# Kernel tuning notes

Hardware: AMD Instinct MI355X
Metric: run time of the kernel (lower is better)

## Reference

```python
import jax, jax.numpy as jnp
import numpy as np

N_NODES = 50000
N_EDGES = 800000
IN_DIM = 128
HID = 128
N_GRAPHS = 256
N_CLASSES = 2
ALPHA = 0.2  # leaky relu slope
EPS_BN = 1e-5


def setup_inputs() -> dict:
    key = jax.random.key(0)
    ks = jax.random.split(key, 24)
    adjacency = jax.random.randint(ks[0], (2, N_EDGES), 0, N_NODES, dtype=jnp.int32)
    input_feature = jax.random.normal(ks[1], (N_NODES, IN_DIM), dtype=jnp.float32)
    graph_indicator = jnp.sort(jax.random.randint(ks[2], (N_NODES,), 0, N_GRAPHS, dtype=jnp.int32))
    labels = jax.random.randint(ks[3], (N_GRAPHS,), 0, N_CLASSES, dtype=jnp.int64)
    s = 0.05
    params = {
        'W1': jax.random.normal(ks[4], (IN_DIM, HID), jnp.float32) * s,
        'a1': jax.random.normal(ks[5], (2 * HID,), jnp.float32) * s,
        'bn2_g': jnp.ones((HID,), jnp.float32),
        'bn2_b': jnp.zeros((HID,), jnp.float32),
        'W2': jax.random.normal(ks[6], (HID, HID), jnp.float32) * s,
        'a2': jax.random.normal(ks[7], (2 * HID,), jnp.float32) * s,
        'bn3_g': jnp.ones((HID,), jnp.float32),
        'bn3_b': jnp.zeros((HID,), jnp.float32),
        'W3': jax.random.normal(ks[8], (HID, HID), jnp.float32) * s,
        'a3': jax.random.normal(ks[9], (2 * HID,), jnp.float32) * s,
        'fc1_w': jax.random.normal(ks[10], (HID, 2 * HID), jnp.float32) * s,
        'fc1_b': jnp.zeros((2 * HID,), jnp.float32),
        'fc2_w': jax.random.normal(ks[11], (2 * HID, HID), jnp.float32) * s,
        'fc2_b': jnp.zeros((HID,), jnp.float32),
        'fc3_w': jax.random.normal(ks[12], (HID, N_CLASSES), jnp.float32) * s,
        'fc3_b': jnp.zeros((N_CLASSES,), jnp.float32),
    }
    return dict(adjacency=adjacency, input_feature=input_feature,
                graph_indicator=graph_indicator, labels=labels, **params)


def _batchnorm(x, g, b):
    # training-mode BatchNorm1d over node dim (biased variance)
    mu = jnp.mean(x, axis=0)
    var = jnp.mean((x - mu) ** 2, axis=0)
    return (x - mu) * jax.lax.rsqrt(var + EPS_BN) * g + b


def _sp_gat(x, src, dst, W, a):
    # pyGAT SpGraphAttentionLayer (dropout disabled / eval mode)
    h = x @ W                                # [N, F]
    F = h.shape[1]
    e_src = h @ a[:F]                        # [N]
    e_dst = h @ a[F:]                        # [N]
    e = e_src[src] + e_dst[dst]              # [E]
    ee = jnp.exp(-jax.nn.leaky_relu(e, ALPHA))
    rowsum = jax.ops.segment_sum(ee, src, num_segments=N_NODES)          # [N]
    num = jax.ops.segment_sum(ee[:, None] * h[dst], src, num_segments=N_NODES)  # [N, F]
    h_prime = num / (rowsum[:, None] + 1e-16)
    return jax.nn.elu(h_prime)


def reference(adjacency, input_feature, graph_indicator, labels,
              W1, a1, bn2_g, bn2_b, W2, a2, bn3_g, bn3_b, W3, a3,
              fc1_w, fc1_b, fc2_w, fc2_b, fc3_w, fc3_b):
    src, dst = adjacency[0], adjacency[1]
    # bn1 output is discarded in the original forward
    x = _sp_gat(input_feature, src, dst, W1, a1)
    x = _batchnorm(x, bn2_g, bn2_b)
    x = _sp_gat(x, src, dst, W2, a2)
    x = _batchnorm(x, bn3_g, bn3_b)
    x = _sp_gat(x, src, dst, W3, a3)
    # pooling_sum_4tensor: per-graph sum pooling
    pooled = jax.ops.segment_sum(x, graph_indicator, num_segments=N_GRAPHS)  # [G, F]
    x = jax.nn.relu(pooled @ fc1_w + fc1_b)
    x = jax.nn.relu(x @ fc2_w + fc2_b)
    logits = x @ fc3_w + fc3_b
    return logits
```

## Files before the change

kernel.cpp:

```cpp
#include <hip/hip_runtime.h>
#include <hip/hip_bf16.h>

#define N_NODES 50000
#define N_EDGES 800000
#define FD 128
#define N_GRAPHS 256
#define NPART 6250

typedef unsigned short u16;
typedef short bf16x8 __attribute__((ext_vector_type(8)));
typedef float f32x4 __attribute__((ext_vector_type(4)));

__device__ __forceinline__ u16 f2bf(float v) {
    __hip_bfloat16 h = __float2bfloat16(v);
    union { __hip_bfloat16 hh; u16 u; } c; c.hh = h; return c.u;
}
__device__ __forceinline__ float bf2f(u16 r) {
    return __uint_as_float(((unsigned int)r) << 16);
}

__global__ __launch_bounds__(256) void count_deg_part_k(const int* __restrict__ src,
                                                        int* __restrict__ cnt, int E) {
    int part = blockIdx.x & 7;
    int lo = part * NPART, hi = lo + NPART;
    int stride = (gridDim.x >> 3) * 256;
    for (int e = (blockIdx.x >> 3) * 256 + threadIdx.x; e < E; e += stride) {
        int s = src[e];
        if (s >= lo && s < hi) atomicAdd(&cnt[s], 1);
    }
}

__global__ __launch_bounds__(256) void fill_csr_part_k(const int* __restrict__ src,
                                                       const int* __restrict__ dst,
                                                       int* __restrict__ cur,
                                                       int* __restrict__ edst, int E) {
    int part = blockIdx.x & 7;
    int lo = part * NPART, hi = lo + NPART;
    int stride = (gridDim.x >> 3) * 256;
    for (int e = (blockIdx.x >> 3) * 256 + threadIdx.x; e < E; e += stride) {
        int s = src[e];
        if (s >= lo && s < hi) {
            int p = atomicAdd(&cur[s], 1);
            edst[p] = dst[e];
        }
    }
}

__global__ __launch_bounds__(256) void scan1_k(const int* __restrict__ cnt,
                                               int* __restrict__ bsum, int M,
                                               float* __restrict__ bnbuf,
                                               float* __restrict__ pooled) {
    int i = blockIdx.x * 256 + threadIdx.x;
    int v = (i < M) ? cnt[i] : 0;
    __shared__ int l[256];
    l[threadIdx.x] = v;
    __syncthreads();
    for (int s = 128; s > 0; s >>= 1) {
        if (threadIdx.x < s) l[threadIdx.x] += l[threadIdx.x + s];
        __syncthreads();
    }
    if (threadIdx.x == 0) bsum[blockIdx.x] = l[0];
    if (blockIdx.x == 0) {
        bnbuf[threadIdx.x] = 0.f; bnbuf[threadIdx.x + 256] = 0.f;
        for (int k = threadIdx.x; k < N_GRAPHS * FD; k += 256) pooled[k] = 0.f;
    }
}

__global__ __launch_bounds__(256) void scan3_k(const int* __restrict__ cnt,
                                               const int* __restrict__ bsum,
                                               int* __restrict__ offs,
                                               int* __restrict__ cur, int M, int NB) {
    int i = blockIdx.x * 256 + threadIdx.x;
    int tid = threadIdx.x;
    __shared__ int bs[256];
    bs[tid] = (tid < NB) ? bsum[tid] : 0;
    __syncthreads();
    for (int off = 1; off < 256; off <<= 1) {
        int t = (tid >= off) ? bs[tid - off] : 0;
        __syncthreads();
        bs[tid] += t;
        __syncthreads();
    }
    int base = (blockIdx.x == 0) ? 0 : bs[blockIdx.x - 1];
    int v = (i < M) ? cnt[i] : 0;
    __shared__ int l[256];
    l[tid] = v;
    __syncthreads();
    for (int off = 1; off < 256; off <<= 1) {
        int t = (tid >= off) ? l[tid - off] : 0;
        __syncthreads();
        l[tid] += t;
        __syncthreads();
    }
    int excl = l[tid] - v + base;
    if (i < M) { offs[i] = excl; cur[i] = excl; }
    if (i == M - 1) offs[M] = excl + v;
}

__global__ __launch_bounds__(128) void wprep1_k(const float* __restrict__ W,
                                                u16* __restrict__ Wt,
                                                float* __restrict__ cvec) {
    int n = blockIdx.x, k = threadIdx.x;
    Wt[(size_t)n * FD + k] = f2bf(W[(size_t)k * FD + n]);
    if (k == 0) cvec[n] = 0.f;
}

__global__ __launch_bounds__(128) void bnfw_k(const float* __restrict__ W,
                                              const float* __restrict__ sums,
                                              const float* __restrict__ sumsq,
                                              const float* __restrict__ g,
                                              const float* __restrict__ b,
                                              float invN,
                                              u16* __restrict__ Wt,
                                              float* __restrict__ cvec) {
    int n = blockIdx.x, k = threadIdx.x;
    __shared__ float scs[128], shs[128], l[128];
    float mu = sums[k] * invN;
    float var = sumsq[k] * invN - mu * mu;
    float sc = g[k] * rsqrtf(var + 1e-5f);
    scs[k] = sc;
    shs[k] = b[k] - mu * sc;
    __syncthreads();
    float w = W[(size_t)k * FD + n];
    Wt[(size_t)n * FD + k] = f2bf(scs[k] * w);
    l[k] = shs[k] * w;
    __syncthreads();
    for (int s = 64; s > 0; s >>= 1) {
        if (k < s) l[k] += l[k + s];
        __syncthreads();
    }
    if (k == 0) cvec[n] = l[0];
}

__global__ __launch_bounds__(256) void gemm_mfma_k(const float* __restrict__ Xf,
                                                   const u16* __restrict__ Xb,
                                                   int use_f32,
                                                   const u16* __restrict__ Wt,
                                                   const float* __restrict__ cvec,
                                                   const float* __restrict__ avec,
                                                   u16* __restrict__ Hb,
                                                   float* __restrict__ es,
                                                   float* __restrict__ ed, int M) {
    __shared__ u16 As[64][136];
    __shared__ u16 Bs[128][136];
    __shared__ float sa_s[128], sa_d[128], cv[128];
    int tid = threadIdx.x;
    if (tid < 128) { sa_s[tid] = avec[tid]; sa_d[tid] = avec[128 + tid]; cv[tid] = cvec[tid]; }
    int row0 = blockIdx.x * 64;
    {
        int n = tid >> 1, k0 = (tid & 1) * 64;
        const uint4* s = (const uint4*)(Wt + (size_t)n * FD + k0);
#pragma unroll
        for (int u = 0; u < 8; u++) *(uint4*)&Bs[n][k0 + u * 8] = s[u];
    }
    {
        int r = tid >> 2, k0 = (tid & 3) * 32;
        int grow = row0 + r;
        if (grow < M) {
            if (use_f32) {
                const float4* s = (const float4*)(Xf + (size_t)grow * FD + k0);
#pragma unroll
                for (int u = 0; u < 8; u++) {
                    float4 v = s[u];
                    ushort4 o;
                    o.x = f2bf(v.x); o.y = f2bf(v.y); o.z = f2bf(v.z); o.w = f2bf(v.w);
                    *(ushort4*)&As[r][k0 + u * 4] = o;
                }
            } else {
                const uint4* s = (const uint4*)(Xb + (size_t)grow * FD + k0);
#pragma unroll
                for (int u = 0; u < 4; u++) *(uint4*)&As[r][k0 + u * 8] = s[u];
            }
        } else {
            uint4 z = make_uint4(0, 0, 0, 0);
#pragma unroll
            for (int u = 0; u < 4; u++) *(uint4*)&As[r][k0 + u * 8] = z;
        }
    }
    __syncthreads();

    int wave = tid >> 6, lane = tid & 63;
    int quad = lane >> 4, n16 = lane & 15;
    int rbase = wave * 16;
    f32x4 acc[8];
    f32x4 zz = {0.f, 0.f, 0.f, 0.f};
#pragma unroll
    for (int t = 0; t < 8; t++) acc[t] = zz;

#pragma unroll
    for (int kk = 0; kk < 128; kk += 32) {
        bf16x8 a = *(const bf16x8*)&As[rbase + n16][kk + quad * 8];
#pragma unroll
        for (int t = 0; t < 8; t++) {
            bf16x8 b = *(const bf16x8*)&Bs[t * 16 + n16][kk + quad * 8];
            acc[t] = __builtin_amdgcn_mfma_f32_16x16x32_bf16(a, b, acc[t], 0, 0, 0);
        }
    }

#pragma unroll
    for (int reg = 0; reg < 4; reg++) {
        int grow = row0 + rbase + quad * 4 + reg;
        float vals[8];
        float ps = 0.f, pd = 0.f;
#pragma unroll
        for (int t = 0; t < 8; t++) {
            float v = acc[t][reg] + cv[t * 16 + n16];
            vals[t] = v;
            ps += v * sa_s[t * 16 + n16];
            pd += v * sa_d[t * 16 + n16];
        }
#pragma unroll
        for (int o = 8; o > 0; o >>= 1) { ps += __shfl_xor(ps, o); pd += __shfl_xor(pd, o); }
        if (grow < M) {
            if (n16 == 0) { es[grow] = ps; ed[grow] = pd; }
#pragma unroll
            for (int t = 0; t < 8; t++)
                Hb[(size_t)grow * FD + t * 16 + n16] = f2bf(vals[t]);
        }
    }
}

__global__ __launch_bounds__(256) void agg_k(const u16* __restrict__ Hb,
                                             const float* __restrict__ es_,
                                             const float* __restrict__ ed_,
                                             const int* __restrict__ offs,
                                             const int* __restrict__ edst,
                                             u16* __restrict__ Out, int M) {
    int node = __builtin_amdgcn_readfirstlane((int)((blockIdx.x * blockDim.x + threadIdx.x) >> 6));
    int lane = threadIdx.x & 63;
    if (node >= M) return;
    int s0 = offs[node], s1 = offs[node + 1];
    float esv = es_[node];
    const unsigned int* Hrow = (const unsigned int*)Hb;
    float2 a0 = make_float2(0.f, 0.f), a1 = make_float2(0.f, 0.f);
    float2 a2 = make_float2(0.f, 0.f), a3 = make_float2(0.f, 0.f);
    float rs = 0.f;
    int e = s0;
    for (; e + 8 <= s1; e += 8) {
        int d0 = __builtin_amdgcn_readfirstlane(edst[e]);
        int d1 = __builtin_amdgcn_readfirstlane(edst[e + 1]);
        int d2 = __builtin_amdgcn_readfirstlane(edst[e + 2]);
        int d3 = __builtin_amdgcn_readfirstlane(edst[e + 3]);
        int d4 = __builtin_amdgcn_readfirstlane(edst[e + 4]);
        int d5 = __builtin_amdgcn_readfirstlane(edst[e + 5]);
        int d6 = __builtin_amdgcn_readfirstlane(edst[e + 6]);
        int d7 = __builtin_amdgcn_readfirstlane(edst[e + 7]);
        float w0, w1, w2, w3, w4, w5, w6, w7;
        {
            float ev = esv + ed_[d0]; float lr = ev > 0.f ? ev : 0.2f * ev; w0 = __expf(-lr);
        }
        { float ev = esv + ed_[d1]; float lr = ev > 0.f ? ev : 0.2f * ev; w1 = __expf(-lr); }
        { float ev = esv + ed_[d2]; float lr = ev > 0.f ? ev : 0.2f * ev; w2 = __expf(-lr); }
        { float ev = esv + ed_[d3]; float lr = ev > 0.f ? ev : 0.2f * ev; w3 = __expf(-lr); }
        { float ev = esv + ed_[d4]; float lr = ev > 0.f ? ev : 0.2f * ev; w4 = __expf(-lr); }
        { float ev = esv + ed_[d5]; float lr = ev > 0.f ? ev : 0.2f * ev; w5 = __expf(-lr); }
        { float ev = esv + ed_[d6]; float lr = ev > 0.f ? ev : 0.2f * ev; w6 = __expf(-lr); }
        { float ev = esv + ed_[d7]; float lr = ev > 0.f ? ev : 0.2f * ev; w7 = __expf(-lr); }
        unsigned int r0 = Hrow[(size_t)d0 * 64 + lane];
        unsigned int r1 = Hrow[(size_t)d1 * 64 + lane];
        unsigned int r2 = Hrow[(size_t)d2 * 64 + lane];
        unsigned int r3 = Hrow[(size_t)d3 * 64 + lane];
        unsigned int r4 = Hrow[(size_t)d4 * 64 + lane];
        unsigned int r5 = Hrow[(size_t)d5 * 64 + lane];
        unsigned int r6 = Hrow[(size_t)d6 * 64 + lane];
        unsigned int r7 = Hrow[(size_t)d7 * 64 + lane];
        rs += w0 + w1 + w2 + w3 + w4 + w5 + w6 + w7;
        a0.x += w0 * __uint_as_float(r0 << 16);
        a0.y += w0 * __uint_as_float(r0 & 0xffff0000u);
        a1.x += w1 * __uint_as_float(r1 << 16);
        a1.y += w1 * __uint_as_float(r1 & 0xffff0000u);
        a2.x += w2 * __uint_as_float(r2 << 16);
        a2.y += w2 * __uint_as_float(r2 & 0xffff0000u);
        a3.x += w3 * __uint_as_float(r3 << 16);
        a3.y += w3 * __uint_as_float(r3 & 0xffff0000u);
        a0.x += w4 * __uint_as_float(r4 << 16);
        a0.y += w4 * __uint_as_float(r4 & 0xffff0000u);
        a1.x += w5 * __uint_as_float(r5 << 16);
        a1.y += w5 * __uint_as_float(r5 & 0xffff0000u);
        a2.x += w6 * __uint_as_float(r6 << 16);
        a2.y += w6 * __uint_as_float(r6 & 0xffff0000u);
        a3.x += w7 * __uint_as_float(r7 << 16);
        a3.y += w7 * __uint_as_float(r7 & 0xffff0000u);
    }
    for (; e < s1; e++) {
        int d = __builtin_amdgcn_readfirstlane(edst[e]);
        float ev = esv + ed_[d];
        float lr = ev > 0.f ? ev : 0.2f * ev;
        float wv = __expf(-lr);
        rs += wv;
        unsigned int r = Hrow[(size_t)d * 64 + lane];
        a0.x += wv * __uint_as_float(r << 16);
        a0.y += wv * __uint_as_float(r & 0xffff0000u);
    }
    float inv = 1.f / (rs + 1e-16f);
    float vx = (a0.x + a1.x + a2.x + a3.x) * inv;
    float vy = (a0.y + a1.y + a2.y + a3.y) * inv;
    vx = vx > 0.f ? vx : (__expf(vx) - 1.f);
    vy = vy > 0.f ? vy : (__expf(vy) - 1.f);
    unsigned int pk = ((unsigned int)f2bf(vy) << 16) | f2bf(vx);
    ((unsigned int*)Out)[(size_t)node * 64 + lane] = pk;
}

__global__ void bnstats_b_k(const u16* __restrict__ Xb, float* __restrict__ sums,
                            float* __restrict__ sumsq, int M) {
    int f = threadIdx.x & 127;
    int half = threadIdx.x >> 7;
    float s1 = 0.f, s2 = 0.f;
    for (int r = blockIdx.x * 2 + half; r < M; r += gridDim.x * 2) {
        float v = bf2f(Xb[(size_t)r * FD + f]);
        s1 += v; s2 += v * v;
    }
    __shared__ float l1[256], l2[256];
    l1[threadIdx.x] = s1; l2[threadIdx.x] = s2;
    __syncthreads();
    if (half == 0) {
        atomicAdd(&sums[f], l1[f] + l1[f + 128]);
        atomicAdd(&sumsq[f], l2[f] + l2[f + 128]);
    }
}

__global__ void pool_k(const u16* __restrict__ Xb, const int* __restrict__ gi,
                       float* __restrict__ pooled, int M) {
    int f = threadIdx.x & 127;
    int half = threadIdx.x >> 7;
    int r0 = blockIdx.x * 128 + half;
    int rend = min(blockIdx.x * 128 + 128, M);
    int curg = -1; float acc = 0.f;
    for (int r = r0; r < rend; r += 2) {
        int g = gi[r];
        if (g != curg) {
            if (curg >= 0) atomicAdd(&pooled[(size_t)curg * FD + f], acc);
            curg = g; acc = 0.f;
        }
        acc += bf2f(Xb[(size_t)r * FD + f]);
    }
    if (curg >= 0) atomicAdd(&pooled[(size_t)curg * FD + f], acc);
}

__global__ __launch_bounds__(256) void mlp_k(const float* __restrict__ pooled,
                                             const float* __restrict__ fc1w, const float* __restrict__ fc1b,
                                             const float* __restrict__ fc2w, const float* __restrict__ fc2b,
                                             const float* __restrict__ fc3w, const float* __restrict__ fc3b,
                                             float* __restrict__ out) {
    int g = blockIdx.x, j = threadIdx.x;
    __shared__ float x[128], t1[256], t2[128], p0[128], p1[128];
    if (j < 128) x[j] = pooled[(size_t)g * FD + j];
    __syncthreads();
    float s = fc1b[j];
    for (int k = 0; k < 128; k++) s += x[k] * fc1w[(size_t)k * 256 + j];
    t1[j] = fmaxf(s, 0.f);
    __syncthreads();
    if (j < 128) {
        float s2 = fc2b[j];
        for (int k = 0; k < 256; k++) s2 += t1[k] * fc2w[(size_t)k * 128 + j];
        t2[j] = fmaxf(s2, 0.f);
    }
    __syncthreads();
    if (j < 128) { p0[j] = t2[j] * fc3w[j * 2]; p1[j] = t2[j] * fc3w[j * 2 + 1]; }
    __syncthreads();
    for (int s3 = 64; s3 > 0; s3 >>= 1) {
        if (j < s3) { p0[j] += p0[j + s3]; p1[j] += p1[j + s3]; }
        __syncthreads();
    }
    if (j == 0) { out[g * 2] = p0[0] + fc3b[0]; out[g * 2 + 1] = p1[0] + fc3b[1]; }
}

extern "C" void kernel_launch(void* const* d_in, const int* in_sizes, int n_in,
                              void* d_out, int out_size, void* d_ws, size_t ws_size,
                              hipStream_t stream) {
    const int*   adj  = (const int*)d_in[0];
    const float* xin  = (const float*)d_in[1];
    const int*   gi   = (const int*)d_in[2];
    const float* W1   = (const float*)d_in[4];
    const float* a1   = (const float*)d_in[5];
    const float* bn2g = (const float*)d_in[6];
    const float* bn2b = (const float*)d_in[7];
    const float* W2   = (const float*)d_in[8];
    const float* a2   = (const float*)d_in[9];
    const float* bn3g = (const float*)d_in[10];
    const float* bn3b = (const float*)d_in[11];
    const float* W3   = (const float*)d_in[12];
    const float* a3   = (const float*)d_in[13];
    const float* fc1w = (const float*)d_in[14];
    const float* fc1b = (const float*)d_in[15];
    const float* fc2w = (const float*)d_in[16];
    const float* fc2b = (const float*)d_in[17];
    const float* fc3w = (const float*)d_in[18];
    const float* fc3b = (const float*)d_in[19];
    float* out = (float*)d_out;

    const int N = N_NODES, E = N_EDGES, G = N_GRAPHS;

    u16*   Xb     = (u16*)d_ws;
    u16*   Hb     = Xb + (size_t)N * FD;
    u16*   Wt     = Hb + (size_t)N * FD;
    float* es     = (float*)(Wt + FD * FD);
    float* ed     = es + N;
    float* bnbuf  = ed + N;
    float* sumsA  = bnbuf;
    float* sumsqA = bnbuf + 128;
    float* sumsB  = bnbuf + 256;
    float* sumsqB = bnbuf + 384;
    float* cvec   = bnbuf + 512;
    float* pooled = cvec + FD;
    int*   degcnt = (int*)(pooled + (size_t)G * FD);
    int*   offs   = degcnt + N;
    int*   cur    = offs + (N + 2);
    int*   bsum   = cur + N;
    int*   edst   = bsum + 256;

    const int* srcp = adj;
    const int* dstp = adj + E;

    const int NB = (N + 255) / 256;

    hipMemsetAsync(degcnt, 0, (size_t)N * sizeof(int), stream);
    count_deg_part_k<<<8 * 392, 256, 0, stream>>>(srcp, degcnt, E);
    scan1_k<<<NB, 256, 0, stream>>>(degcnt, bsum, N, bnbuf, pooled);
    scan3_k<<<NB, 256, 0, stream>>>(degcnt, bsum, offs, cur, N, NB);
    fill_csr_part_k<<<8 * 392, 256, 0, stream>>>(srcp, dstp, cur, edst, E);

    const int gemm_grid = (N + 63) / 64;
    const int wave_grid = (N + 3) / 4;
    const float invN = 1.0f / (float)N;

    wprep1_k<<<FD, 128, 0, stream>>>(W1, Wt, cvec);
    gemm_mfma_k<<<gemm_grid, 256, 0, stream>>>(xin, Xb, 1, Wt, cvec, a1, Hb, es, ed, N);
    agg_k<<<wave_grid, 256, 0, stream>>>(Hb, es, ed, offs, edst, Xb, N);
    bnstats_b_k<<<256, 256, 0, stream>>>(Xb, sumsA, sumsqA, N);

    bnfw_k<<<FD, 128, 0, stream>>>(W2, sumsA, sumsqA, bn2g, bn2b, invN, Wt, cvec);
    gemm_mfma_k<<<gemm_grid, 256, 0, stream>>>(nullptr, Xb, 0, Wt, cvec, a2, Hb, es, ed, N);
    agg_k<<<wave_grid, 256, 0, stream>>>(Hb, es, ed, offs, edst, Xb, N);
    bnstats_b_k<<<256, 256, 0, stream>>>(Xb, sumsB, sumsqB, N);

    bnfw_k<<<FD, 128, 0, stream>>>(W3, sumsB, sumsqB, bn3g, bn3b, invN, Wt, cvec);
    gemm_mfma_k<<<gemm_grid, 256, 0, stream>>>(nullptr, Xb, 0, Wt, cvec, a3, Hb, es, ed, N);
    agg_k<<<wave_grid, 256, 0, stream>>>(Hb, es, ed, offs, edst, Xb, N);

    pool_k<<<(N + 127) / 128, 256, 0, stream>>>(Xb, gi, pooled, N);
    mlp_k<<<G, 256, 0, stream>>>(pooled, fc1w, fc1b, fc2w, fc2b, fc3w, fc3b, out);
}
```

Before: 426.3 us.

## Fuse weight prep into GEMM, lane-parallel edge weights, pooling into final aggregation

Removes the separate weight-transpose/BN-fold kernels by having every GEMM block fold the batchnorm scale and shift into its own bf16 copy of W, and drops pool_k by having the last aggregation atomically add node outputs into per-graph sums. In the aggregation, edge indices and attention weights are now loaded and exponentiated once per lane for up to 64 edges, then broadcast with readlane, instead of each wave redundantly computing them per edge. The cost is that every GEMM block repeats the small 128x128 weight transform, and the pooling now issues many fp32 atomics contending on 256 graph rows.

```diff
diff --git a/kernel.cpp b/kernel.cpp
--- a/kernel.cpp
+++ b/kernel.cpp
@@ -17,6 +17,9 @@
 }
 __device__ __forceinline__ float bf2f(u16 r) {
     return __uint_as_float(((unsigned int)r) << 16);
+}
+__device__ __forceinline__ float rdlane_f(float v, int l) {
+    return __uint_as_float((unsigned int)__builtin_amdgcn_readlane((int)__float_as_uint(v), l));
 }
 
 __global__ __launch_bounds__(256) void count_deg_part_k(const int* __restrict__ src,
@@ -97,62 +100,58 @@
     if (i == M - 1) offs[M] = excl + v;
 }
 
-__global__ __launch_bounds__(128) void wprep1_k(const float* __restrict__ W,
-                                                u16* __restrict__ Wt,
-                                                float* __restrict__ cvec) {
-    int n = blockIdx.x, k = threadIdx.x;
-    Wt[(size_t)n * FD + k] = f2bf(W[(size_t)k * FD + n]);
-    if (k == 0) cvec[n] = 0.f;
-}
-
-__global__ __launch_bounds__(128) void bnfw_k(const float* __restrict__ W,
-                                              const float* __restrict__ sums,
-                                              const float* __restrict__ sumsq,
-                                              const float* __restrict__ g,
-                                              const float* __restrict__ b,
-                                              float invN,
-                                              u16* __restrict__ Wt,
-                                              float* __restrict__ cvec) {
-    int n = blockIdx.x, k = threadIdx.x;
-    __shared__ float scs[128], shs[128], l[128];
-    float mu = sums[k] * invN;
-    float var = sumsq[k] * invN - mu * mu;
-    float sc = g[k] * rsqrtf(var + 1e-5f);
-    scs[k] = sc;
-    shs[k] = b[k] - mu * sc;
-    __syncthreads();
-    float w = W[(size_t)k * FD + n];
-    Wt[(size_t)n * FD + k] = f2bf(scs[k] * w);
-    l[k] = shs[k] * w;
-    __syncthreads();
-    for (int s = 64; s > 0; s >>= 1) {
-        if (k < s) l[k] += l[k + s];
-        __syncthreads();
-    }
-    if (k == 0) cvec[n] = l[0];
-}
-
 __global__ __launch_bounds__(256) void gemm_mfma_k(const float* __restrict__ Xf,
                                                    const u16* __restrict__ Xb,
                                                    int use_f32,
-                                                   const u16* __restrict__ Wt,
-                                                   const float* __restrict__ cvec,
+                                                   const float* __restrict__ W,
+                                                   const float* __restrict__ sums,
+                                                   const float* __restrict__ sumsq,
+                                                   const float* __restrict__ g,
+                                                   const float* __restrict__ b,
+                                                   float invN, int haveBN,
                                                    const float* __restrict__ avec,
                                                    u16* __restrict__ Hb,
                                                    float* __restrict__ es,
                                                    float* __restrict__ ed, int M) {
     __shared__ u16 As[64][136];
     __shared__ u16 Bs[128][136];
-    __shared__ float sa_s[128], sa_d[128], cv[128];
+    __shared__ float cv[128];
+    __shared__ float scsh[256];
     int tid = threadIdx.x;
-    if (tid < 128) { sa_s[tid] = avec[tid]; sa_d[tid] = avec[128 + tid]; cv[tid] = cvec[tid]; }
     int row0 = blockIdx.x * 64;
-    {
-        int n = tid >> 1, k0 = (tid & 1) * 64;
-        const uint4* s = (const uint4*)(Wt + (size_t)n * FD + k0);
-#pragma unroll
-        for (int u = 0; u < 8; u++) *(uint4*)&Bs[n][k0 + u * 8] = s[u];
-    }
+
+    if (haveBN) {
+        if (tid < 128) {
+            float mu = sums[tid] * invN;
+            float var = sumsq[tid] * invN - mu * mu;
+            float sc = g[tid] * rsqrtf(var + 1e-5f);
+            scsh[tid] = sc;
+            scsh[128 + tid] = b[tid] - mu * sc;
+        }
+        __syncthreads();
+        float cvp = 0.f;
+#pragma unroll 8
+        for (int i = 0; i < 64; i++) {
+            int idx = i * 256 + tid;
+            int k = idx >> 7;
+            int n = idx & 127;
+            float wv = W[idx];
+            Bs[n][k] = f2bf(scsh[k] * wv);
+            cvp += scsh[128 + k] * wv;
+        }
+        __syncthreads();
+        scsh[tid] = cvp;
+        __syncthreads();
+        if (tid < 128) cv[tid] = scsh[tid] + scsh[tid + 128];
+    } else {
+#pragma unroll 8
+        for (int i = 0; i < 64; i++) {
+            int idx = i * 256 + tid;
+            Bs[idx & 127][idx >> 7] = f2bf(W[idx]);
+        }
+        if (tid < 128) cv[tid] = 0.f;
+    }
+
     {
         int r = tid >> 2, k0 = (tid & 3) * 32;
         int grow = row0 + r;
@@ -192,9 +191,16 @@
         bf16x8 a = *(const bf16x8*)&As[rbase + n16][kk + quad * 8];
 #pragma unroll
         for (int t = 0; t < 8; t++) {
-            bf16x8 b = *(const bf16x8*)&Bs[t * 16 + n16][kk + quad * 8];
-            acc[t] = __builtin_amdgcn_mfma_f32_16x16x32_bf16(a, b, acc[t], 0, 0, 0);
-        }
+            bf16x8 bb = *(const bf16x8*)&Bs[t * 16 + n16][kk + quad * 8];
+            acc[t] = __builtin_amdgcn_mfma_f32_16x16x32_bf16(a, bb, acc[t], 0, 0, 0);
+        }
+    }
+
+    float sas[8], sad[8];
+#pragma unroll
+    for (int t = 0; t < 8; t++) {
+        sas[t] = avec[t * 16 + n16];
+        sad[t] = avec[128 + t * 16 + n16];
     }
 
 #pragma unroll
@@ -206,8 +212,8 @@
         for (int t = 0; t < 8; t++) {
             float v = acc[t][reg] + cv[t * 16 + n16];
             vals[t] = v;
-            ps += v * sa_s[t * 16 + n16];
-            pd += v * sa_d[t * 16 + n16];
+            ps += v * sas[t];
+            pd += v * sad[t];
         }
 #pragma unroll
         for (int o = 8; o > 0; o >>= 1) { ps += __shfl_xor(ps, o); pd += __shfl_xor(pd, o); }
@@ -225,7 +231,10 @@
                                              const float* __restrict__ ed_,
                                              const int* __restrict__ offs,
                                              const int* __restrict__ edst,
-                                             u16* __restrict__ Out, int M) {
+                                             u16* __restrict__ Out,
+                                             const int* __restrict__ gi,
+                                             float* __restrict__ pooled,
+                                             int M) {
     int node = __builtin_amdgcn_readfirstlane((int)((blockIdx.x * blockDim.x + threadIdx.x) >> 6));
     int lane = threadIdx.x & 63;
     if (node >= M) return;
@@ -234,71 +243,90 @@
     const unsigned int* Hrow = (const unsigned int*)Hb;
     float2 a0 = make_float2(0.f, 0.f), a1 = make_float2(0.f, 0.f);
     float2 a2 = make_float2(0.f, 0.f), a3 = make_float2(0.f, 0.f);
-    float rs = 0.f;
-    int e = s0;
-    for (; e + 8 <= s1; e += 8) {
-        int d0 = __builtin_amdgcn_readfirstlane(edst[e]);
-        int d1 = __builtin_amdgcn_readfirstlane(edst[e + 1]);
-        int d2 = __builtin_amdgcn_readfirstlane(edst[e + 2]);
-        int d3 = __builtin_amdgcn_readfirstlane(edst[e + 3]);
-        int d4 = __builtin_amdgcn_readfirstlane(edst[e + 4]);
-        int d5 = __builtin_amdgcn_readfirstlane(edst[e + 5]);
-        int d6 = __builtin_amdgcn_readfirstlane(edst[e + 6]);
-        int d7 = __builtin_amdgcn_readfirstlane(edst[e + 7]);
-        float w0, w1, w2, w3, w4, w5, w6, w7;
-        {
-            float ev = esv + ed_[d0]; float lr = ev > 0.f ? ev : 0.2f * ev; w0 = __expf(-lr);
-        }
-        { float ev = esv + ed_[d1]; float lr = ev > 0.f ? ev : 0.2f * ev; w1 = __expf(-lr); }
-        { float ev = esv + ed_[d2]; float lr = ev > 0.f ? ev : 0.2f * ev; w2 = __expf(-lr); }
-        { float ev = esv + ed_[d3]; float lr = ev > 0.f ? ev : 0.2f * ev; w3 = __expf(-lr); }
-        { float ev = esv + ed_[d4]; float lr = ev > 0.f ? ev : 0.2f * ev; w4 = __expf(-lr); }
-        { float ev = esv + ed_[d5]; float lr = ev > 0.f ? ev : 0.2f * ev; w5 = __expf(-lr); }
-        { float ev = esv + ed_[d6]; float lr = ev > 0.f ? ev : 0.2f * ev; w6 = __expf(-lr); }
-        { float ev = esv + ed_[d7]; float lr = ev > 0.f ? ev : 0.2f * ev; w7 = __expf(-lr); }
-        unsigned int r0 = Hrow[(size_t)d0 * 64 + lane];
-        unsigned int r1 = Hrow[(size_t)d1 * 64 + lane];
-        unsigned int r2 = Hrow[(size_t)d2 * 64 + lane];
-        unsigned int r3 = Hrow[(size_t)d3 * 64 + lane];
-        unsigned int r4 = Hrow[(size_t)d4 * 64 + lane];
-        unsigned int r5 = Hrow[(size_t)d5 * 64 + lane];
-        unsigned int r6 = Hrow[(size_t)d6 * 64 + lane];
-        unsigned int r7 = Hrow[(size_t)d7 * 64 + lane];
-        rs += w0 + w1 + w2 + w3 + w4 + w5 + w6 + w7;
-        a0.x += w0 * __uint_as_float(r0 << 16);
-        a0.y += w0 * __uint_as_float(r0 & 0xffff0000u);
-        a1.x += w1 * __uint_as_float(r1 << 16);
-        a1.y += w1 * __uint_as_float(r1 & 0xffff0000u);
-        a2.x += w2 * __uint_as_float(r2 << 16);
-        a2.y += w2 * __uint_as_float(r2 & 0xffff0000u);
-        a3.x += w3 * __uint_as_float(r3 << 16);
-        a3.y += w3 * __uint_as_float(r3 & 0xffff0000u);
-        a0.x += w4 * __uint_as_float(r4 << 16);
-        a0.y += w4 * __uint_as_float(r4 & 0xffff0000u);
-        a1.x += w5 * __uint_as_float(r5 << 16);
-        a1.y += w5 * __uint_as_float(r5 & 0xffff0000u);
-        a2.x += w6 * __uint_as_float(r6 << 16);
-        a2.y += w6 * __uint_as_float(r6 & 0xffff0000u);
-        a3.x += w7 * __uint_as_float(r7 << 16);
-        a3.y += w7 * __uint_as_float(r7 & 0xffff0000u);
-    }
-    for (; e < s1; e++) {
-        int d = __builtin_amdgcn_readfirstlane(edst[e]);
-        float ev = esv + ed_[d];
-        float lr = ev > 0.f ? ev : 0.2f * ev;
-        float wv = __expf(-lr);
-        rs += wv;
-        unsigned int r = Hrow[(size_t)d * 64 + lane];
-        a0.x += wv * __uint_as_float(r << 16);
-        a0.y += wv * __uint_as_float(r & 0xffff0000u);
-    }
+    float rsl = 0.f;
+    for (int base = s0; base < s1; base += 64) {
+        int rem = s1 - base;
+        int nE = rem < 64 ? rem : 64;
+        int dv = 0; float wv = 0.f;
+        if (lane < nE) {
+            dv = edst[base + lane];
+            float ev = esv + ed_[dv];
+            float lr = ev > 0.f ? ev : 0.2f * ev;
+            wv = __expf(-lr);
+        }
+        rsl += wv;
+        int j = 0;
+        for (; j + 8 <= nE; j += 8) {
+            int d0 = __builtin_amdgcn_readlane(dv, j + 0);
+            int d1 = __builtin_amdgcn_readlane(dv, j + 1);
+            int d2 = __builtin_amdgcn_readlane(dv, j + 2);
+            int d3 = __builtin_amdgcn_readlane(dv, j + 3);
+            int d4 = __builtin_amdgcn_readlane(dv, j + 4);
+            int d5 = __builtin_amdgcn_readlane(dv, j + 5);
+            int d6 = __builtin_amdgcn_readlane(dv, j + 6);
+            int d7 = __builtin_amdgcn_readlane(dv, j + 7);
+            float w0 = rdlane_f(wv, j + 0);
+            float w1 = rdlane_f(wv, j + 1);
+            float w2 = rdlane_f(wv, j + 2);
+            float w3 = rdlane_f(wv, j + 3);
+            float w4 = rdlane_f(wv, j + 4);
+            float w5 = rdlane_f(wv, j + 5);
+            float w6 = rdlane_f(wv, j + 6);
+            float w7 = rdlane_f(wv, j + 7);
+            unsigned int r0 = Hrow[(size_t)d0 * 64 + lane];
+            unsigned int r1 = Hrow[(size_t)d1 * 64 + lane];
+            unsigned int r2 = Hrow[(size_t)d2 * 64 + lane];
+            unsigned int r3 = Hrow[(size_t)d3 * 64 + lane];
+            unsigned int r4 = Hrow[(size_t)d4 * 64 + lane];
+            unsigned int r5 = Hrow[(size_t)d5 * 64 + lane];
+            unsigned int r6 = Hrow[(size_t)d6 * 64 + lane];
+            unsigned int r7 = Hrow[(size_t)d7 * 64 + lane];
+            a0.x += w0 * __uint_as_float(r0 << 16);
+            a0.y += w0 * __uint_as_float(r0 & 0xffff0000u);
+            a1.x += w1 * __uint_as_float(r1 << 16);
+            a1.y += w1 * __uint_as_float(r1 & 0xffff0000u);
+            a2.x += w2 * __uint_as_float(r2 << 16);
+            a2.y += w2 * __uint_as_float(r2 & 0xffff0000u);
+            a3.x += w3 * __uint_as_float(r3 << 16);
+            a3.y += w3 * __uint_as_float(r3 & 0xffff0000u);
+            a0.x += w4 * __uint_as_float(r4 << 16);
+            a0.y += w4 * __uint_as_float(r4 & 0xffff0000u);
+            a1.x += w5 * __uint_as_float(r5 << 16);
+            a1.y += w5 * __uint_as_float(r5 & 0xffff0000u);
+            a2.x += w6 * __uint_as_float(r6 << 16);
+            a2.y += w6 * __uint_as_float(r6 & 0xffff0000u);
+            a3.x += w7 * __uint_as_float(r7 << 16);
+            a3.y += w7 * __uint_as_float(r7 & 0xffff0000u);
+        }
+        for (; j < nE; j++) {
+            int d = __builtin_amdgcn_readlane(dv, j);
+            float wj = rdlane_f(wv, j);
+            unsigned int r = Hrow[(size_t)d * 64 + lane];
+            if (j & 1) {
+                a1.x += wj * __uint_as_float(r << 16);
+                a1.y += wj * __uint_as_float(r & 0xffff0000u);
+            } else {
+                a0.x += wj * __uint_as_float(r << 16);
+                a0.y += wj * __uint_as_float(r & 0xffff0000u);
+            }
+        }
+    }
+    float rs = rsl;
+#pragma unroll
+    for (int o = 32; o > 0; o >>= 1) rs += __shfl_xor(rs, o);
     float inv = 1.f / (rs + 1e-16f);
     float vx = (a0.x + a1.x + a2.x + a3.x) * inv;
     float vy = (a0.y + a1.y + a2.y + a3.y) * inv;
     vx = vx > 0.f ? vx : (__expf(vx) - 1.f);
     vy = vy > 0.f ? vy : (__expf(vy) - 1.f);
-    unsigned int pk = ((unsigned int)f2bf(vy) << 16) | f2bf(vx);
-    ((unsigned int*)Out)[(size_t)node * 64 + lane] = pk;
+    if (pooled) {
+        int gg = __builtin_amdgcn_readfirstlane(gi[node]);
+        atomicAdd(&pooled[(size_t)gg * FD + 2 * lane], vx);
+        atomicAdd(&pooled[(size_t)gg * FD + 2 * lane + 1], vy);
+    } else {
+        unsigned int pk = ((unsigned int)f2bf(vy) << 16) | f2bf(vx);
+        ((unsigned int*)Out)[(size_t)node * 64 + lane] = pk;
+    }
 }
 
 __global__ void bnstats_b_k(const u16* __restrict__ Xb, float* __restrict__ sums,
@@ -317,24 +345,6 @@
         atomicAdd(&sums[f], l1[f] + l1[f + 128]);
         atomicAdd(&sumsq[f], l2[f] + l2[f + 128]);
     }
-}
-
-__global__ void pool_k(const u16* __restrict__ Xb, const int* __restrict__ gi,
-                       float* __restrict__ pooled, int M) {
-    int f = threadIdx.x & 127;
-    int half = threadIdx.x >> 7;
-    int r0 = blockIdx.x * 128 + half;
-    int rend = min(blockIdx.x * 128 + 128, M);
-    int curg = -1; float acc = 0.f;
-    for (int r = r0; r < rend; r += 2) {
-        int g = gi[r];
-        if (g != curg) {
-            if (curg >= 0) atomicAdd(&pooled[(size_t)curg * FD + f], acc);
-            curg = g; acc = 0.f;
-        }
-        acc += bf2f(Xb[(size_t)r * FD + f]);
-    }
-    if (curg >= 0) atomicAdd(&pooled[(size_t)curg * FD + f], acc);
 }
 
 __global__ __launch_bounds__(256) void mlp_k(const float* __restrict__ pooled,
@@ -424,20 +434,22 @@
     const int wave_grid = (N + 3) / 4;
     const float invN = 1.0f / (float)N;
 
-    wprep1_k<<<FD, 128, 0, stream>>>(W1, Wt, cvec);
-    gemm_mfma_k<<<gemm_grid, 256, 0, stream>>>(xin, Xb, 1, Wt, cvec, a1, Hb, es, ed, N);
-    agg_k<<<wave_grid, 256, 0, stream>>>(Hb, es, ed, offs, edst, Xb, N);
+    gemm_mfma_k<<<gemm_grid, 256, 0, stream>>>(xin, Xb, 1, W1,
+                                               nullptr, nullptr, nullptr, nullptr, invN, 0,
+                                               a1, Hb, es, ed, N);
+    agg_k<<<wave_grid, 256, 0, stream>>>(Hb, es, ed, offs, edst, Xb, nullptr, nullptr, N);
     bnstats_b_k<<<256, 256, 0, stream>>>(Xb, sumsA, sumsqA, N);
 
-    bnfw_k<<<FD, 128, 0, stream>>>(W2, sumsA, sumsqA, bn2g, bn2b, invN, Wt, cvec);
-    gemm_mfma_k<<<gemm_grid, 256, 0, stream>>>(nullptr, Xb, 0, Wt, cvec, a2, Hb, es, ed, N);
-    agg_k<<<wave_grid, 256, 0, stream>>>(Hb, es, ed, offs, edst, Xb, N);
+    gemm_mfma_k<<<gemm_grid, 256, 0, stream>>>(nullptr, Xb, 0, W2,
+                                               sumsA, sumsqA, bn2g, bn2b, invN, 1,
+                                               a2, Hb, es, ed, N);
+    agg_k<<<wave_grid, 256, 0, stream>>>(Hb, es, ed, offs, edst, Xb, nullptr, nullptr, N);
     bnstats_b_k<<<256, 256, 0, stream>>>(Xb, sumsB, sumsqB, N);
 
-    bnfw_k<<<FD, 128, 0, stream>>>(W3, sumsB, sumsqB, bn3g, bn3b, invN, Wt, cvec);
-    gemm_mfma_k<<<gemm_grid, 256, 0, stream>>>(nullptr, Xb, 0, Wt, cvec, a3, Hb, es, ed, N);
-    agg_k<<<wave_grid, 256, 0, stream>>>(Hb, es, ed, offs, edst, Xb, N);
-
-    pool_k<<<(N + 127) / 128, 256, 0, stream>>>(Xb, gi, pooled, N);
+    gemm_mfma_k<<<gemm_grid, 256, 0, stream>>>(nullptr, Xb, 0, W3,
+                                               sumsB, sumsqB, bn3g, bn3b, invN, 1,
+                                               a3, Hb, es, ed, N);
+    agg_k<<<wave_grid, 256, 0, stream>>>(Hb, es, ed, offs, edst, nullptr, gi, pooled, N);
+
     mlp_k<<<G, 256, 0, stream>>>(pooled, fc1w, fc1b, fc2w, fc2b, fc3w, fc3b, out);
 }
```

Result: slower. 442.2 us (+3.7%).
